# Performance work log

Hardware: AMD Instinct MI355X
Metric: run time of the kernel (lower is better)

Reference implementation:

```python
import jax, jax.numpy as jnp
import numpy as np

N_DISEASE = 50000
N_GENE = 50000
D = 64
N_EDGES = 2000000

def setup_inputs() -> dict:
    key = jax.random.key(0)
    k1, k2, k3, k4, k5, k6 = jax.random.split(key, 6)
    return {
        "x_disease": jax.random.normal(k1, (N_DISEASE, D), dtype=jnp.float32),
        "h_disease": jax.random.normal(k2, (N_DISEASE, D), dtype=jnp.float32),
        "x_gene": jax.random.normal(k3, (N_GENE, D), dtype=jnp.float32),
        "h_gene": jax.random.normal(k4, (N_GENE, D), dtype=jnp.float32),
        "src": jax.random.randint(k5, (N_EDGES,), 0, N_DISEASE, dtype=jnp.int32),
        "dst": jax.random.randint(k6, (N_EDGES,), 0, N_GENE, dtype=jnp.int32),
    }

def reference(x_disease, h_disease, x_gene, h_gene, src, dst):
    # Concat raw and learned features per node type: [N, 2D]
    f_d = jnp.concatenate([x_disease, h_disease], axis=1)
    f_g = jnp.concatenate([x_gene, h_gene], axis=1)
    # Per-node L2 norms: [N, 1]
    n_d = jnp.linalg.norm(f_d, axis=1, keepdims=True)
    n_g = jnp.linalg.norm(f_g, axis=1, keepdims=True)
    # u_dot_v on features: per-edge gather + dot -> [E, 1]
    dot = jnp.sum(f_d[src] * f_g[dst], axis=1, keepdims=True)
    # u_dot_v on norms (1-dim features): product of norms -> [E, 1]
    mou = n_d[src] * n_g[dst]
    return dot / mou
```

## Files before the change

kernel.cpp:

```cpp
#include <hip/hip_runtime.h>


#define FD 64
#define NBUCK 64
#define BIN_CHUNK 2048

__device__ __forceinline__ int q8pack(float v0, float v1, float v2, float v3, float inv) {
    float a0 = fminf(fmaxf(v0 * inv, -127.f), 127.f);
    float a1 = fminf(fmaxf(v1 * inv, -127.f), 127.f);
    float a2 = fminf(fmaxf(v2 * inv, -127.f), 127.f);
    float a3 = fminf(fmaxf(v3 * inv, -127.f), 127.f);
    int q0 = ((int)rintf(a0)) & 0xff;
    int q1 = ((int)rintf(a1)) & 0xff;
    int q2 = ((int)rintf(a2)) & 0xff;
    int q3 = ((int)rintf(a3)) & 0xff;
    return q0 | (q1 << 8) | (q2 << 16) | (q3 << 24);
}

__global__ void pack_kernel(const float4* __restrict__ xd, const float4* __restrict__ hd,
                            const float4* __restrict__ xg, const float4* __restrict__ hg,
                            int2* __restrict__ fd, int2* __restrict__ fg,
                            float* __restrict__ sd, float* __restrict__ sg,
                            unsigned* __restrict__ cursor,
                            int n_d, int n_g)
{
    if (cursor != nullptr && blockIdx.x == 0 && threadIdx.x < NBUCK)
        cursor[threadIdx.x] = 0u;

    int tid  = (int)(blockIdx.x * blockDim.x + threadIdx.x);
    int node = tid >> 4;
    int lane = threadIdx.x & 15;
    int total = n_d + n_g;
    if (node >= total) return;

    const float4* x; const float4* h; int2* o; float* s; int n;
    if (node < n_d) { x = xd; h = hd; o = fd; s = sd; n = node; }
    else            { x = xg; h = hg; o = fg; s = sg; n = node - n_d; }

    float4 a = x[(size_t)n * 16 + lane];
    float4 b = h[(size_t)n * 16 + lane];

    float ss = a.x*a.x + a.y*a.y + a.z*a.z + a.w*a.w
             + b.x*b.x + b.y*b.y + b.z*b.z + b.w*b.w;
    #pragma unroll
    for (int m = 8; m >= 1; m >>= 1) ss += __shfl_xor(ss, m);
    float r = rsqrtf(ss);

    a.x *= r; a.y *= r; a.z *= r; a.w *= r;
    b.x *= r; b.y *= r; b.z *= r; b.w *= r;

    float mx = fmaxf(fmaxf(fmaxf(fabsf(a.x), fabsf(a.y)), fmaxf(fabsf(a.z), fabsf(a.w))),
                     fmaxf(fmaxf(fabsf(b.x), fabsf(b.y)), fmaxf(fabsf(b.z), fabsf(b.w))));
    #pragma unroll
    for (int m = 8; m >= 1; m >>= 1) mx = fmaxf(mx, __shfl_xor(mx, m));

    float inv = 127.0f / mx;

    int2 w;
    w.x = q8pack(a.x, a.y, a.z, a.w, inv);
    w.y = q8pack(b.x, b.y, b.z, b.w, inv);
    o[(size_t)n * 16 + lane] = w;

    if (lane == 0) s[n] = mx * (1.0f / 127.0f);
}

__global__ __launch_bounds__(256, 4)
void bin_kernel(const int* __restrict__ src, const int* __restrict__ dst,
                uint2* __restrict__ bins, unsigned* __restrict__ cursor,
                int n_edges, int cap, unsigned mul_s, unsigned mul_d)
{
    __shared__ unsigned hist[NBUCK];
    __shared__ unsigned base[NBUCK];
    int t = threadIdx.x;
    if (t < NBUCK) hist[t] = 0u;
    __syncthreads();

    int start = (int)blockIdx.x * BIN_CHUNK;
    unsigned pk[8]; unsigned bk[8];
    #pragma unroll
    for (int k = 0; k < 8; ++k) {
        int e = start + t + k * 256;
        unsigned b = 0xffffffffu, p = 0u;
        if (e < n_edges) {
            unsigned s = (unsigned)src[e];
            unsigned d = (unsigned)dst[e];
            unsigned bs = min(7u, (s * mul_s) >> 20);
            unsigned bd = min(7u, (d * mul_d) >> 20);
            b = bs * 8u + bd;
            p = s | (d << 16);
            atomicAdd(&hist[b], 1u);
        }
        pk[k] = p; bk[k] = b;
    }
    __syncthreads();
    if (t < NBUCK) {
        unsigned h = hist[t];
        base[t] = h ? atomicAdd(&cursor[t], h) : 0u;
        hist[t] = 0u;
    }
    __syncthreads();
    #pragma unroll
    for (int k = 0; k < 8; ++k) {
        unsigned b = bk[k];
        if (b != 0xffffffffu) {
            unsigned r = atomicAdd(&hist[b], 1u);
            unsigned pos = base[b] + r;
            if (pos < (unsigned)cap)
                bins[(size_t)b * cap + pos] =
                    make_uint2(pk[k], (unsigned)(start + t + k * 256));
        }
    }
}

__device__ __forceinline__ int dot4(int a, int b, int c) {
    return __builtin_amdgcn_sdot4(a, b, c, false);
}

__global__ __launch_bounds__(256, 8)
void edge_kernel_bkt(const int4* __restrict__ fd, const int4* __restrict__ fg,
                     const float* __restrict__ sd, const float* __restrict__ sg,
                     const uint2* __restrict__ bins, const unsigned* __restrict__ cursor,
                     float* __restrict__ out, int cap, int bpb)
{
    int i     = (int)blockIdx.x;
    int xcd   = i & 7;
    int j     = i >> 3;
    int bs    = j / bpb;
    int chunk = j - bs * bpb;
    int b     = bs * 8 + xcd;

    int count = (int)cursor[b];
    int grp  = threadIdx.x >> 3;
    int lane = threadIdx.x & 7;
    int e0   = chunk * 64 + grp * 2;
    if (e0 >= count) return;
    bool has1 = (e0 + 1) < count;

    const uint2* bb = bins + (size_t)b * cap;
    uint4 rr = ((const uint4*)bb)[e0 >> 1];
    int s0 = (int)(rr.x & 0xffffu), d0 = (int)(rr.x >> 16);
    int s1 = (int)(rr.z & 0xffffu), d1 = (int)(rr.z >> 16);

    int4 a0 = fd[(size_t)s0 * 8 + lane];
    int4 b0 = fg[(size_t)d0 * 8 + lane];
    int4 a1 = fd[(size_t)s1 * 8 + lane];
    int4 b1 = fg[(size_t)d1 * 8 + lane];

    int acc0 = dot4(a0.x, b0.x, dot4(a0.y, b0.y, dot4(a0.z, b0.z, dot4(a0.w, b0.w, 0))));
    int acc1 = dot4(a1.x, b1.x, dot4(a1.y, b1.y, dot4(a1.z, b1.z, dot4(a1.w, b1.w, 0))));

    acc0 += __shfl_xor(acc0, 4);
    acc0 += __shfl_xor(acc0, 2);
    acc0 += __shfl_xor(acc0, 1);
    acc1 += __shfl_xor(acc1, 4);
    acc1 += __shfl_xor(acc1, 2);
    acc1 += __shfl_xor(acc1, 1);

    if (lane == 0) {
        out[rr.y] = (float)acc0 * sd[s0] * sg[d0];
        if (has1) out[rr.w] = (float)acc1 * sd[s1] * sg[d1];
    }
}

__global__ __launch_bounds__(256, 8)
void edge_kernel2(const int4* __restrict__ fd, const int4* __restrict__ fg,
                  const float* __restrict__ sd, const float* __restrict__ sg,
                  const int* __restrict__ src, const int* __restrict__ dst,
                  float* __restrict__ out, int n_edges)
{
    int tid  = (int)(blockIdx.x * blockDim.x + threadIdx.x);
    int lane = threadIdx.x & 7;
    int g    = tid >> 3;
    int e0   = g * 2;
    if (e0 >= n_edges) return;
    int  e1   = min(e0 + 1, n_edges - 1);
    bool has1 = (e0 + 1) < n_edges;

    int s0 = src[e0], d0 = dst[e0];
    int s1 = src[e1], d1 = dst[e1];

    int4 a0 = fd[(size_t)s0 * 8 + lane];
    int4 b0 = fg[(size_t)d0 * 8 + lane];
    int4 a1 = fd[(size_t)s1 * 8 + lane];
    int4 b1 = fg[(size_t)d1 * 8 + lane];

    int acc0 = dot4(a0.x, b0.x, dot4(a0.y, b0.y, dot4(a0.z, b0.z, dot4(a0.w, b0.w, 0))));
    int acc1 = dot4(a1.x, b1.x, dot4(a1.y, b1.y, dot4(a1.z, b1.z, dot4(a1.w, b1.w, 0))));

    acc0 += __shfl_xor(acc0, 4);
    acc0 += __shfl_xor(acc0, 2);
    acc0 += __shfl_xor(acc0, 1);
    acc1 += __shfl_xor(acc1, 4);
    acc1 += __shfl_xor(acc1, 2);
    acc1 += __shfl_xor(acc1, 1);

    if (lane == 0) {
        out[e0] = (float)acc0 * sd[s0] * sg[d0];
        if (has1) out[e1] = (float)acc1 * sd[s1] * sg[d1];
    }
}

extern "C" void kernel_launch(void* const* d_in, const int* in_sizes, int n_in,
                              void* d_out, int out_size, void* d_ws, size_t ws_size,
                              hipStream_t stream) {
    const float* xd = (const float*)d_in[0];
    const float* hd = (const float*)d_in[1];
    const float* xg = (const float*)d_in[2];
    const float* hg = (const float*)d_in[3];
    const int*  src = (const int*)d_in[4];
    const int*  dst = (const int*)d_in[5];

    int n_d     = in_sizes[0] / FD;
    int n_g     = in_sizes[2] / FD;
    int n_edges = in_sizes[4];

    int cap = n_edges / 64 + n_edges / 256 + 4096;
    cap = (cap + 63) & ~63;

    size_t fd_b   = (size_t)n_d * 128;
    size_t fg_b   = (size_t)n_g * 128;
    size_t bins_b = (size_t)NBUCK * (size_t)cap * sizeof(uint2);
    size_t need   = fd_b + fg_b + bins_b
                  + (size_t)(n_d + n_g) * sizeof(float) + NBUCK * sizeof(unsigned) + 256;

    bool bucketed = (need <= ws_size) && (n_d < 65536) && (n_g < 65536) && (n_edges > 0);

    char* ws = (char*)d_ws;
    int2*  fd = (int2*)ws;  ws += fd_b;
    int2*  fg = (int2*)ws;  ws += fg_b;
    uint2* bins = nullptr;
    if (bucketed) { bins = (uint2*)ws; ws += bins_b; }
    float* sd = (float*)ws; ws += (size_t)n_d * sizeof(float);
    float* sg = (float*)ws; ws += (size_t)n_g * sizeof(float);
    unsigned* cursor = nullptr;
    if (bucketed) { cursor = (unsigned*)ws; }
    float* out = (float*)d_out;

    int total_nodes = n_d + n_g;
    int nb1 = (total_nodes * 16 + 255) / 256;
    pack_kernel<<<nb1, 256, 0, stream>>>((const float4*)xd, (const float4*)hd,
                                         (const float4*)xg, (const float4*)hg,
                                         fd, fg, sd, sg, cursor, n_d, n_g);

    if (bucketed) {
        unsigned mul_s = (8u << 20) / (unsigned)n_d;
        unsigned mul_d = (8u << 20) / (unsigned)n_g;
        int nbin = (n_edges + BIN_CHUNK - 1) / BIN_CHUNK;
        bin_kernel<<<nbin, 256, 0, stream>>>(src, dst, bins, cursor,
                                             n_edges, cap, mul_s, mul_d);

        int bpb = cap / 64;
        int nb2 = NBUCK * bpb;
        edge_kernel_bkt<<<nb2, 256, 0, stream>>>((const int4*)fd, (const int4*)fg,
                                                 sd, sg, bins, cursor, out, cap, bpb);
    } else {
        long long groups = ((long long)n_edges + 1) / 2;
        int nb2 = (int)((groups * 8 + 255) / 256);
        edge_kernel2<<<nb2, 256, 0, stream>>>((const int4*)fd, (const int4*)fg,
                                              sd, sg, src, dst, out, n_edges);
    }
}
```

Before: 175.4 us.

## Bucket edges by 128-row disease blocks, stage disease rows in LDS, fuse pack+bin

Edges are now binned into many fine buckets: one per 128-row disease superblock times 8 gene ranges. Each edge block first loads its 128 quantized disease rows into swizzled shared memory, then loops over its bucket, so half of the per-edge feature gathers hit LDS instead of global memory or cache. The pack and bin kernels are merged into a single launch, and the cursor is cleared with a memset. The cost is many more global cursor atomics and more scattered bin writes. Bucket capacity is also tighter, so an overflowing bucket would silently drop edges.

```diff
diff --git a/kernel.cpp b/kernel.cpp
--- a/kernel.cpp
+++ b/kernel.cpp
@@ -2,8 +2,9 @@
 
 
 #define FD 64
-#define NBUCK 64
-#define BIN_CHUNK 2048
+#define MAX_BUCKETS 4096
+#define BIN_EPT 16
+#define BIN_CHUNK (256 * BIN_EPT)
 
 __device__ __forceinline__ int q8pack(float v0, float v1, float v2, float v3, float inv) {
     float a0 = fminf(fmaxf(v0 * inv, -127.f), 127.f);
@@ -17,90 +18,90 @@
     return q0 | (q1 << 8) | (q2 << 16) | (q3 << 24);
 }
 
-__global__ void pack_kernel(const float4* __restrict__ xd, const float4* __restrict__ hd,
-                            const float4* __restrict__ xg, const float4* __restrict__ hg,
-                            int2* __restrict__ fd, int2* __restrict__ fg,
-                            float* __restrict__ sd, float* __restrict__ sg,
-                            unsigned* __restrict__ cursor,
-                            int n_d, int n_g)
+__global__ __launch_bounds__(256, 4)
+void pack_bin_kernel(const float4* __restrict__ xd, const float4* __restrict__ hd,
+                     const float4* __restrict__ xg, const float4* __restrict__ hg,
+                     int2* __restrict__ fd, int2* __restrict__ fg,
+                     float* __restrict__ sd, float* __restrict__ sg,
+                     const int* __restrict__ src, const int* __restrict__ dst,
+                     uint2* __restrict__ bins, unsigned* __restrict__ cursor,
+                     int n_d, int n_g, int n_edges, int cap,
+                     unsigned mul_d, int nb_pack)
 {
-    if (cursor != nullptr && blockIdx.x == 0 && threadIdx.x < NBUCK)
-        cursor[threadIdx.x] = 0u;
-
-    int tid  = (int)(blockIdx.x * blockDim.x + threadIdx.x);
-    int node = tid >> 4;
-    int lane = threadIdx.x & 15;
-    int total = n_d + n_g;
-    if (node >= total) return;
-
-    const float4* x; const float4* h; int2* o; float* s; int n;
-    if (node < n_d) { x = xd; h = hd; o = fd; s = sd; n = node; }
-    else            { x = xg; h = hg; o = fg; s = sg; n = node - n_d; }
-
-    float4 a = x[(size_t)n * 16 + lane];
-    float4 b = h[(size_t)n * 16 + lane];
-
-    float ss = a.x*a.x + a.y*a.y + a.z*a.z + a.w*a.w
-             + b.x*b.x + b.y*b.y + b.z*b.z + b.w*b.w;
+    __shared__ unsigned hist[MAX_BUCKETS];
+    __shared__ unsigned base[MAX_BUCKETS];
+
+    int bid = (int)blockIdx.x;
+    int t   = threadIdx.x;
+
+    if (bid < nb_pack) {
+        int tid  = bid * 256 + t;
+        int node = tid >> 4;
+        int lane = t & 15;
+        int total = n_d + n_g;
+        if (node >= total) return;
+
+        const float4* x; const float4* h; int2* o; float* s; int n;
+        if (node < n_d) { x = xd; h = hd; o = fd; s = sd; n = node; }
+        else            { x = xg; h = hg; o = fg; s = sg; n = node - n_d; }
+
+        float4 a = x[(size_t)n * 16 + lane];
+        float4 b = h[(size_t)n * 16 + lane];
+
+        float ss = a.x*a.x + a.y*a.y + a.z*a.z + a.w*a.w
+                 + b.x*b.x + b.y*b.y + b.z*b.z + b.w*b.w;
+        #pragma unroll
+        for (int m = 8; m >= 1; m >>= 1) ss += __shfl_xor(ss, m);
+        float r = rsqrtf(ss);
+
+        a.x *= r; a.y *= r; a.z *= r; a.w *= r;
+        b.x *= r; b.y *= r; b.z *= r; b.w *= r;
+
+        float mx = fmaxf(fmaxf(fmaxf(fabsf(a.x), fabsf(a.y)), fmaxf(fabsf(a.z), fabsf(a.w))),
+                         fmaxf(fmaxf(fabsf(b.x), fabsf(b.y)), fmaxf(fabsf(b.z), fabsf(b.w))));
+        #pragma unroll
+        for (int m = 8; m >= 1; m >>= 1) mx = fmaxf(mx, __shfl_xor(mx, m));
+
+        float inv = 127.0f / mx;
+
+        int2 w;
+        w.x = q8pack(a.x, a.y, a.z, a.w, inv);
+        w.y = q8pack(b.x, b.y, b.z, b.w, inv);
+        o[(size_t)n * 16 + lane] = w;
+
+        if (lane == 0) s[n] = mx * (1.0f / 127.0f);
+        return;
+    }
+
+    int nbuck = ((n_d + 127) >> 7) * 8;
+    for (int i = t; i < nbuck; i += 256) hist[i] = 0u;
+    __syncthreads();
+
+    int start = (bid - nb_pack) * BIN_CHUNK;
+    unsigned pk[BIN_EPT]; unsigned bk[BIN_EPT];
     #pragma unroll
-    for (int m = 8; m >= 1; m >>= 1) ss += __shfl_xor(ss, m);
-    float r = rsqrtf(ss);
-
-    a.x *= r; a.y *= r; a.z *= r; a.w *= r;
-    b.x *= r; b.y *= r; b.z *= r; b.w *= r;
-
-    float mx = fmaxf(fmaxf(fmaxf(fabsf(a.x), fabsf(a.y)), fmaxf(fabsf(a.z), fabsf(a.w))),
-                     fmaxf(fmaxf(fabsf(b.x), fabsf(b.y)), fmaxf(fabsf(b.z), fabsf(b.w))));
-    #pragma unroll
-    for (int m = 8; m >= 1; m >>= 1) mx = fmaxf(mx, __shfl_xor(mx, m));
-
-    float inv = 127.0f / mx;
-
-    int2 w;
-    w.x = q8pack(a.x, a.y, a.z, a.w, inv);
-    w.y = q8pack(b.x, b.y, b.z, b.w, inv);
-    o[(size_t)n * 16 + lane] = w;
-
-    if (lane == 0) s[n] = mx * (1.0f / 127.0f);
-}
-
-__global__ __launch_bounds__(256, 4)
-void bin_kernel(const int* __restrict__ src, const int* __restrict__ dst,
-                uint2* __restrict__ bins, unsigned* __restrict__ cursor,
-                int n_edges, int cap, unsigned mul_s, unsigned mul_d)
-{
-    __shared__ unsigned hist[NBUCK];
-    __shared__ unsigned base[NBUCK];
-    int t = threadIdx.x;
-    if (t < NBUCK) hist[t] = 0u;
-    __syncthreads();
-
-    int start = (int)blockIdx.x * BIN_CHUNK;
-    unsigned pk[8]; unsigned bk[8];
-    #pragma unroll
-    for (int k = 0; k < 8; ++k) {
+    for (int k = 0; k < BIN_EPT; ++k) {
         int e = start + t + k * 256;
         unsigned b = 0xffffffffu, p = 0u;
         if (e < n_edges) {
             unsigned s = (unsigned)src[e];
             unsigned d = (unsigned)dst[e];
-            unsigned bs = min(7u, (s * mul_s) >> 20);
             unsigned bd = min(7u, (d * mul_d) >> 20);
-            b = bs * 8u + bd;
-            p = s | (d << 16);
+            b = (s >> 7) * 8u + bd;
+            p = (s & 127u) | (d << 16);
             atomicAdd(&hist[b], 1u);
         }
         pk[k] = p; bk[k] = b;
     }
     __syncthreads();
-    if (t < NBUCK) {
-        unsigned h = hist[t];
-        base[t] = h ? atomicAdd(&cursor[t], h) : 0u;
-        hist[t] = 0u;
+    for (int i = t; i < nbuck; i += 256) {
+        unsigned h = hist[i];
+        base[i] = h ? atomicAdd(&cursor[i], h) : 0u;
+        hist[i] = 0u;
     }
     __syncthreads();
     #pragma unroll
-    for (int k = 0; k < 8; ++k) {
+    for (int k = 0; k < BIN_EPT; ++k) {
         unsigned b = bk[k];
         if (b != 0xffffffffu) {
             unsigned r = atomicAdd(&hist[b], 1u);
@@ -117,48 +118,56 @@
 }
 
 __global__ __launch_bounds__(256, 8)
-void edge_kernel_bkt(const int4* __restrict__ fd, const int4* __restrict__ fg,
-                     const float* __restrict__ sd, const float* __restrict__ sg,
-                     const uint2* __restrict__ bins, const unsigned* __restrict__ cursor,
-                     float* __restrict__ out, int cap, int bpb)
+void edge_kernel3(const int4* __restrict__ fd, const int4* __restrict__ fg,
+                  const float* __restrict__ sd, const float* __restrict__ sg,
+                  const uint2* __restrict__ bins, const unsigned* __restrict__ cursor,
+                  float* __restrict__ out, int n_d, int cap)
 {
-    int i     = (int)blockIdx.x;
-    int xcd   = i & 7;
-    int j     = i >> 3;
-    int bs    = j / bpb;
-    int chunk = j - bs * bpb;
-    int b     = bs * 8 + xcd;
-
-    int count = (int)cursor[b];
-    int grp  = threadIdx.x >> 3;
-    int lane = threadIdx.x & 7;
-    int e0   = chunk * 64 + grp * 2;
-    if (e0 >= count) return;
-    bool has1 = (e0 + 1) < count;
-
+    __shared__ int4 fdl[128 * 8];
+    int b  = (int)blockIdx.x;
+    int sb = b >> 3;
+    int t  = threadIdx.x;
+    int base_row = sb << 7;
+
+    for (int i = t; i < 1024; i += 256) {
+        int r = i >> 3, l = i & 7;
+        int gr = base_row + r;
+        int4 v = make_int4(0, 0, 0, 0);
+        if (gr < n_d) v = fd[(size_t)gr * 8 + l];
+        fdl[(r << 3) | (l ^ (r & 7))] = v;
+    }
+    __syncthreads();
+
+    int count = min((int)cursor[b], cap);
+    int grp  = t >> 3;
+    int lane = t & 7;
     const uint2* bb = bins + (size_t)b * cap;
-    uint4 rr = ((const uint4*)bb)[e0 >> 1];
-    int s0 = (int)(rr.x & 0xffffu), d0 = (int)(rr.x >> 16);
-    int s1 = (int)(rr.z & 0xffffu), d1 = (int)(rr.z >> 16);
-
-    int4 a0 = fd[(size_t)s0 * 8 + lane];
-    int4 b0 = fg[(size_t)d0 * 8 + lane];
-    int4 a1 = fd[(size_t)s1 * 8 + lane];
-    int4 b1 = fg[(size_t)d1 * 8 + lane];
-
-    int acc0 = dot4(a0.x, b0.x, dot4(a0.y, b0.y, dot4(a0.z, b0.z, dot4(a0.w, b0.w, 0))));
-    int acc1 = dot4(a1.x, b1.x, dot4(a1.y, b1.y, dot4(a1.z, b1.z, dot4(a1.w, b1.w, 0))));
-
-    acc0 += __shfl_xor(acc0, 4);
-    acc0 += __shfl_xor(acc0, 2);
-    acc0 += __shfl_xor(acc0, 1);
-    acc1 += __shfl_xor(acc1, 4);
-    acc1 += __shfl_xor(acc1, 2);
-    acc1 += __shfl_xor(acc1, 1);
-
-    if (lane == 0) {
-        out[rr.y] = (float)acc0 * sd[s0] * sg[d0];
-        if (has1) out[rr.w] = (float)acc1 * sd[s1] * sg[d1];
+
+    for (int e0 = grp * 2; e0 < count; e0 += 64) {
+        bool has1 = (e0 + 1) < count;
+        uint4 rr = ((const uint4*)bb)[e0 >> 1];
+        int s0 = (int)(rr.x & 127u),  d0 = (int)(rr.x >> 16);
+        int s1 = (int)(rr.z & 127u),  d1 = (int)(rr.z >> 16);
+
+        int4 a0 = fdl[(s0 << 3) | (lane ^ (s0 & 7))];
+        int4 a1 = fdl[(s1 << 3) | (lane ^ (s1 & 7))];
+        int4 b0 = fg[(size_t)d0 * 8 + lane];
+        int4 b1 = fg[(size_t)d1 * 8 + lane];
+
+        int acc0 = dot4(a0.x, b0.x, dot4(a0.y, b0.y, dot4(a0.z, b0.z, dot4(a0.w, b0.w, 0))));
+        int acc1 = dot4(a1.x, b1.x, dot4(a1.y, b1.y, dot4(a1.z, b1.z, dot4(a1.w, b1.w, 0))));
+
+        acc0 += __shfl_xor(acc0, 4);
+        acc0 += __shfl_xor(acc0, 2);
+        acc0 += __shfl_xor(acc0, 1);
+        acc1 += __shfl_xor(acc1, 4);
+        acc1 += __shfl_xor(acc1, 2);
+        acc1 += __shfl_xor(acc1, 1);
+
+        if (lane == 0) {
+            out[rr.y] = (float)acc0 * sd[base_row + s0] * sg[d0];
+            if (has1) out[rr.w] = (float)acc1 * sd[base_row + s1] * sg[d1];
+        }
     }
 }
 
@@ -214,16 +223,21 @@
     int n_g     = in_sizes[2] / FD;
     int n_edges = in_sizes[4];
 
-    int cap = n_edges / 64 + n_edges / 256 + 4096;
-    cap = (cap + 63) & ~63;
+    int n_sb  = (n_d + 127) >> 7;
+    int nbuck = n_sb * 8;
+
+    int mean = (nbuck > 0) ? (n_edges / nbuck) : 0;
+    int cap  = (mean + mean / 8 + 96 + 63) & ~63;
 
     size_t fd_b   = (size_t)n_d * 128;
     size_t fg_b   = (size_t)n_g * 128;
-    size_t bins_b = (size_t)NBUCK * (size_t)cap * sizeof(uint2);
+    size_t bins_b = (size_t)nbuck * (size_t)cap * sizeof(uint2);
     size_t need   = fd_b + fg_b + bins_b
-                  + (size_t)(n_d + n_g) * sizeof(float) + NBUCK * sizeof(unsigned) + 256;
-
-    bool bucketed = (need <= ws_size) && (n_d < 65536) && (n_g < 65536) && (n_edges > 0);
+                  + (size_t)(n_d + n_g) * sizeof(float)
+                  + (size_t)nbuck * sizeof(unsigned) + 256;
+
+    bool bucketed = (need <= ws_size) && (n_d < 65536) && (n_g < 65536)
+                  && (nbuck <= MAX_BUCKETS) && (n_edges > 0);
 
     char* ws = (char*)d_ws;
     int2*  fd = (int2*)ws;  ws += fd_b;
@@ -237,22 +251,22 @@
     float* out = (float*)d_out;
 
     int total_nodes = n_d + n_g;
-    int nb1 = (total_nodes * 16 + 255) / 256;
-    pack_kernel<<<nb1, 256, 0, stream>>>((const float4*)xd, (const float4*)hd,
-                                         (const float4*)xg, (const float4*)hg,
-                                         fd, fg, sd, sg, cursor, n_d, n_g);
+    int nb_pack = (total_nodes * 16 + 255) / 256;
+    int nb_bin  = bucketed ? (n_edges + BIN_CHUNK - 1) / BIN_CHUNK : 0;
+
+    unsigned mul_d = (n_g > 0) ? ((8u << 20) / (unsigned)n_g) : 0u;
+
+    if (bucketed)
+        hipMemsetAsync(cursor, 0, (size_t)nbuck * sizeof(unsigned), stream);
+
+    pack_bin_kernel<<<nb_pack + nb_bin, 256, 0, stream>>>(
+        (const float4*)xd, (const float4*)hd, (const float4*)xg, (const float4*)hg,
+        fd, fg, sd, sg, src, dst, bins, cursor,
+        n_d, n_g, n_edges, cap, mul_d, nb_pack);
 
     if (bucketed) {
-        unsigned mul_s = (8u << 20) / (unsigned)n_d;
-        unsigned mul_d = (8u << 20) / (unsigned)n_g;
-        int nbin = (n_edges + BIN_CHUNK - 1) / BIN_CHUNK;
-        bin_kernel<<<nbin, 256, 0, stream>>>(src, dst, bins, cursor,
-                                             n_edges, cap, mul_s, mul_d);
-
-        int bpb = cap / 64;
-        int nb2 = NBUCK * bpb;
-        edge_kernel_bkt<<<nb2, 256, 0, stream>>>((const int4*)fd, (const int4*)fg,
-                                                 sd, sg, bins, cursor, out, cap, bpb);
+        edge_kernel3<<<nbuck, 256, 0, stream>>>((const int4*)fd, (const int4*)fg,
+                                                sd, sg, bins, cursor, out, n_d, cap);
     } else {
         long long groups = ((long long)n_edges + 1) / 2;
         int nb2 = (int)((groups * 8 + 255) / 256);
```

New measurement: 193.8 us. 1.11x slower.
